# Performance work log

Hardware: AMD Instinct MI355X
Metric: run time of the kernel (lower is better)

## Reference

```python
import jax, jax.numpy as jnp
import numpy as np

# Mex config (matches init_kwargs)
B, C, H, W = 64, 64, 64, 64
BLK = (64, 3, 3)        # block over (C, H, W); spans all channels -> out_c = 1
STR = (64, 2, 2)
PAD = (0, 1, 1)
NI = 256                # num_instances
EPS = 1.0
SOFTMAX_MODE = False    # False -> mean (logsumexp - log k), True -> plain logsumexp


def setup_inputs() -> dict:
    key = jax.random.key(0)
    k1, k2 = jax.random.split(key)
    x = jax.random.normal(k1, (B, C, H, W), dtype=jnp.float32)
    kblk = BLK[0] * BLK[1] * BLK[2]
    # Dirichlet([1]*k) init == normalized exponentials; nregions = 1 (shared offsets)
    e = jax.random.exponential(k2, (1, NI, kblk), dtype=jnp.float32)
    offsets = (e / jnp.sum(e, axis=-1, keepdims=True)).reshape(1, NI, *BLK)
    return {"x": x, "offsets": offsets}


def _mex_forward(x, offsets):
    eps = jnp.float32(EPS)
    bc, bh, bw = BLK
    # im2col patch extraction: (B, C*bh*bw, OH, OW); feature dim ordered (c, fh, fw)
    patches = jax.lax.conv_general_dilated_patches(
        x, (bh, bw), (STR[1], STR[2]),
        [(PAD[1], PAD[1]), (PAD[2], PAD[2])],  # zero padding == blocks_out_of_bounds_value
        dimension_numbers=("NCHW", "OIHW", "NCHW"),
    )
    Bn, K, OH, OW = patches.shape  # K = bc*bh*bw = 576
    P = patches.transpose(0, 2, 3, 1).reshape(-1, K)  # (N, k), N = B*OH*OW
    O = offsets.reshape(NI, K)                         # single shared region

    # y_ni = (1/eps) * logsumexp_k( eps*(P_nk + O_ik) ) - log(k)/eps (mean mode)
    # exp-domain GEMM with max-shift for stability:
    Pe = eps * P
    Oe = eps * O
    mp = jnp.max(Pe, axis=1, keepdims=True)   # (N, 1)
    mo = jnp.max(Oe, axis=1, keepdims=True)   # (I, 1)
    S = jnp.exp(Pe - mp) @ jnp.exp(Oe - mo).T  # (N, I)
    y = (jnp.log(S) + mp + mo.T) / eps
    if not SOFTMAX_MODE:
        y = y - jnp.log(jnp.float32(K)) / eps
    # output: (B, num_instances * out_c, OH, OW) with out_c = 1
    return y.reshape(Bn, OH, OW, NI).transpose(0, 3, 1, 2)


def reference(x, offsets):
    return _mex_forward(x, offsets)
```

## Files before the change

### kernel.cpp

```cpp
#include <hip/hip_runtime.h>
#include <hip/hip_bf16.h>


typedef __bf16 bf16x8 __attribute__((ext_vector_type(8)));
typedef float  f32x4  __attribute__((ext_vector_type(4)));

#define GLD16(gp, lp) __builtin_amdgcn_global_load_lds(                        \
    (const __attribute__((address_space(1))) unsigned int*)(gp),               \
    (__attribute__((address_space(3))) unsigned int*)(lp), 16, 0, 0)

__global__ void mex_prep_b(const float* __restrict__ off, __bf16* __restrict__ Bt) {
    const int i = blockIdx.x * 4 + (threadIdx.x >> 6);
    const int c = threadIdx.x & 63;
    const float* oi = off + i * 576;
    __bf16* bi = Bt + i * 576;
    #pragma unroll
    for (int p = 0; p < 9; ++p) {
        float v = oi[c * 9 + p];
        bi[p * 64 + c] = (__bf16)__expf(v);
    }
}

__global__ __launch_bounds__(256) void mex_exp_tr(const float* __restrict__ x,
                                                  __bf16* __restrict__ E) {
    __shared__ __bf16 t[64 * 68];
    const int bh = blockIdx.x;
    const int b  = bh >> 6, h = bh & 63;
    const float* xp = x + ((size_t)b << 18) + (h << 6);
    const int tid = threadIdx.x;

    #pragma unroll
    for (int i = 0; i < 4; ++i) {
        const int f  = tid + i * 256;
        const int c  = f >> 4;
        const int w0 = (f & 15) << 2;
        float4 v = *(const float4*)(xp + c * 4096 + w0);
        __bf16* d = &t[c * 68 + w0];
        d[0] = (__bf16)__expf(v.x);
        d[1] = (__bf16)__expf(v.y);
        d[2] = (__bf16)__expf(v.z);
        d[3] = (__bf16)__expf(v.w);
    }
    __syncthreads();

    __bf16* Erow = E + ((size_t)bh << 12);
    #pragma unroll
    for (int j = 0; j < 2; ++j) {
        const int id = tid + j * 256;
        const int w = id >> 3, c8 = id & 7;
        bf16x8 v;
        #pragma unroll
        for (int ii = 0; ii < 8; ++ii) v[ii] = t[(c8 * 8 + ii) * 68 + w];
        const int c8p = c8 ^ ((w >> 1) & 7);
        *(bf16x8*)(Erow + w * 64 + c8p * 8) = v;
    }
}

__global__ __launch_bounds__(256, 3) void mex_main(
        const __bf16* __restrict__ E,
        const __bf16* __restrict__ Bt,
        float* __restrict__ out) {
    __shared__ bf16x8 lds8[5 * 66 * 8];

    const int bid = blockIdx.x;
    const int b   = bid >> 4;
    const int oh0 = (bid & 15) << 1;
    const int tid  = threadIdx.x;
    const int lane = tid & 63;
    const int wv   = tid >> 6;

    bf16x8 one8;
    #pragma unroll
    for (int j = 0; j < 8; ++j) one8[j] = (__bf16)1.0f;
    if (tid < 40) {
        const int hl = tid >> 3, cc = tid & 7;
        lds8[(hl * 66) * 8 + cc] = one8;
    }
    if (oh0 == 0) {
        for (int i = tid; i < 66 * 8; i += 256) lds8[i] = one8;
    }

    #pragma unroll
    for (int s = 0; s < 10; ++s) {
        const int seg = wv * 10 + s;
        const int hl = seg >> 3, sg = seg & 7;
        const int hg = 2 * oh0 - 1 + hl;
        if (hg >= 0) {
            const __bf16* gp = E + (((size_t)b * 64 + hg) << 12) + (sg << 9) + (lane << 3);
            bf16x8* lp = lds8 + hl * 528 + 8 + sg * 64;
            GLD16(gp, lp);
        }
    }
    __syncthreads();

    const int t16 = tid & 15;
    const int q   = (tid >> 4) & 3;

    int rbase[4], owv[4];
    #pragma unroll
    for (int mt = 0; mt < 4; ++mt) {
        const int m = mt * 16 + t16;
        owv[mt]   = m & 31;
        rbase[mt] = ((m >> 5) * 132) + ((m & 31) * 2);
    }

    const bf16x8* __restrict__ Btv = (const bf16x8*)Bt;
    const int instRow = (wv * 64 + t16) * 72 + q;

    f32x4 acc[4][4];
    #pragma unroll
    for (int mt = 0; mt < 4; ++mt)
        #pragma unroll
        for (int nt = 0; nt < 4; ++nt)
            acc[mt][nt] = (f32x4)(0.0f);

    bf16x8 bcur[4];
    #pragma unroll
    for (int nt = 0; nt < 4; ++nt)
        bcur[nt] = Btv[instRow + nt * (16 * 72)];

    #pragma unroll 2
    for (int ks = 0; ks < 18; ++ks) {
        const int p  = ks >> 1;
        const int fh = (p * 11) >> 5;
        const int fw = p - fh * 3;
        const int rofs = fh * 66 + fw;
        const int ccq  = ((ks & 1) << 2) + q;

        bf16x8 a[4];
        #pragma unroll
        for (int mt = 0; mt < 4; ++mt) {
            const int row = rbase[mt] + rofs;
            const int key = ((owv[mt] * 2 + fw - 1) >> 1) & 7;
            a[mt] = lds8[row * 8 + (ccq ^ key)];
        }

        bf16x8 bnext[4];
        if (ks < 17) {
            #pragma unroll
            for (int nt = 0; nt < 4; ++nt)
                bnext[nt] = Btv[instRow + nt * (16 * 72) + (ks + 1) * 4];
        }

        #pragma unroll
        for (int mt = 0; mt < 4; ++mt)
            #pragma unroll
            for (int nt = 0; nt < 4; ++nt)
                acc[mt][nt] = __builtin_amdgcn_mfma_f32_16x16x32_bf16(
                    a[mt], bcur[nt], acc[mt][nt], 0, 0, 0);

        #pragma unroll
        for (int nt = 0; nt < 4; ++nt) bcur[nt] = bnext[nt];
    }

    const float lK = 6.356107660695891f;
    #pragma unroll
    for (int mt = 0; mt < 4; ++mt) {
        const int m   = mt * 16 + (q << 2);
        const int ohl = m >> 5;
        const int owi = m & 31;
        const int orow = (oh0 + ohl) * 32 + owi;
        #pragma unroll
        for (int nt = 0; nt < 4; ++nt) {
            const int inst = wv * 64 + nt * 16 + t16;
            f32x4 r;
            #pragma unroll
            for (int j = 0; j < 4; ++j)
                r[j] = __logf(acc[mt][nt][j]) - lK;
            *(f32x4*)(out + (((size_t)b * 256 + inst) * 1024 + orow)) = r;
        }
    }
}

extern "C" void kernel_launch(void* const* d_in, const int* in_sizes, int n_in,
                              void* d_out, int out_size, void* d_ws, size_t ws_size,
                              hipStream_t stream) {
    const float* x   = (const float*)d_in[0];
    const float* off = (const float*)d_in[1];
    float* out = (float*)d_out;
    __bf16* E  = (__bf16*)d_ws;
    __bf16* Bt = (__bf16*)((char*)d_ws + 33554432);

    mex_prep_b<<<64, 256, 0, stream>>>(off, Bt);
    mex_exp_tr<<<4096, 256, 0, stream>>>(x, E);
    mex_main<<<1024, 256, 0, stream>>>(E, Bt, out);
}
```

Measured before the change: 157.1 us.

## Drop LDS transpose in exp kernel and swizzle block-to-XCD mapping

The exp/transpose kernel no longer stages data through LDS. Each wave loads eight channel-strided floats per lane, exponentiates them and writes one swizzled bf16x8 vector, on a grid reduced from 4096 to 512 blocks. Both the exp kernel and the main kernel remap block IDs with a (x - b) & 7 rotation over groups of eight, apparently to spread each batch's rows across the XCDs and improve L2 locality for the halo rows the main kernel reads. The main kernel also issues its first B-operand loads before the LDS fill, so those loads overlap the fill. The risk is that the strided 256-byte-per-wave global reads coalesce worse than the old float4 loads.

```diff
diff --git a/kernel.cpp b/kernel.cpp
--- a/kernel.cpp
+++ b/kernel.cpp
@@ -23,36 +23,26 @@
 
 __global__ __launch_bounds__(256) void mex_exp_tr(const float* __restrict__ x,
                                                   __bf16* __restrict__ E) {
-    __shared__ __bf16 t[64 * 68];
-    const int bh = blockIdx.x;
-    const int b  = bh >> 6, h = bh & 63;
-    const float* xp = x + ((size_t)b << 18) + (h << 6);
-    const int tid = threadIdx.x;
+    const int id = blockIdx.x;
+    const int b  = id >> 3;
+    const int g  = (id - b) & 7;
+    const int lane = threadIdx.x & 63;
+    const int wv   = threadIdx.x >> 6;
 
-    #pragma unroll
-    for (int i = 0; i < 4; ++i) {
-        const int f  = tid + i * 256;
-        const int c  = f >> 4;
-        const int w0 = (f & 15) << 2;
-        float4 v = *(const float4*)(xp + c * 4096 + w0);
-        __bf16* d = &t[c * 68 + w0];
-        d[0] = (__bf16)__expf(v.x);
-        d[1] = (__bf16)__expf(v.y);
-        d[2] = (__bf16)__expf(v.z);
-        d[3] = (__bf16)__expf(v.w);
-    }
-    __syncthreads();
-
-    __bf16* Erow = E + ((size_t)bh << 12);
-    #pragma unroll
-    for (int j = 0; j < 2; ++j) {
-        const int id = tid + j * 256;
-        const int w = id >> 3, c8 = id & 7;
-        bf16x8 v;
+    #pragma unroll 4
+    for (int tt = 0; tt < 16; ++tt) {
+        const int task = tt * 4 + wv;
+        const int hh = task >> 3, c8 = task & 7;
+        const int h  = g * 8 + hh;
+        const float* xp = x + (((size_t)(b * 64 + c8 * 8)) << 12) + (h << 6) + lane;
+        float v[8];
         #pragma unroll
-        for (int ii = 0; ii < 8; ++ii) v[ii] = t[(c8 * 8 + ii) * 68 + w];
-        const int c8p = c8 ^ ((w >> 1) & 7);
-        *(bf16x8*)(Erow + w * 64 + c8p * 8) = v;
+        for (int j = 0; j < 8; ++j) v[j] = xp[(size_t)j << 12];
+        bf16x8 o;
+        #pragma unroll
+        for (int j = 0; j < 8; ++j) o[j] = (__bf16)__expf(v[j]);
+        const int c8p = c8 ^ ((lane >> 1) & 7);
+        *(bf16x8*)(E + (((size_t)(b * 64 + h)) << 12) + (lane << 6) + (c8p << 3)) = o;
     }
 }
 
@@ -63,11 +53,25 @@
     __shared__ bf16x8 lds8[5 * 66 * 8];
 
     const int bid = blockIdx.x;
-    const int b   = bid >> 4;
-    const int oh0 = (bid & 15) << 1;
+    const int x8  = bid & 7;
+    const int tt  = bid >> 3;
+    const int b   = tt >> 1;
+    const int e   = tt & 1;
+    const int g   = (x8 - b) & 7;
+    const int oh0 = (g * 2 + e) * 2;
+
     const int tid  = threadIdx.x;
     const int lane = tid & 63;
     const int wv   = tid >> 6;
+    const int t16  = tid & 15;
+    const int q    = (tid >> 4) & 3;
+
+    const bf16x8* __restrict__ Btv = (const bf16x8*)Bt;
+    const int instRow = (wv * 64 + t16) * 72 + q;
+    bf16x8 bcur[4];
+    #pragma unroll
+    for (int nt = 0; nt < 4; ++nt)
+        bcur[nt] = Btv[instRow + nt * (16 * 72)];
 
     bf16x8 one8;
     #pragma unroll
@@ -93,9 +97,6 @@
     }
     __syncthreads();
 
-    const int t16 = tid & 15;
-    const int q   = (tid >> 4) & 3;
-
     int rbase[4], owv[4];
     #pragma unroll
     for (int mt = 0; mt < 4; ++mt) {
@@ -104,20 +105,12 @@
         rbase[mt] = ((m >> 5) * 132) + ((m & 31) * 2);
     }
 
-    const bf16x8* __restrict__ Btv = (const bf16x8*)Bt;
-    const int instRow = (wv * 64 + t16) * 72 + q;
-
     f32x4 acc[4][4];
     #pragma unroll
     for (int mt = 0; mt < 4; ++mt)
         #pragma unroll
         for (int nt = 0; nt < 4; ++nt)
             acc[mt][nt] = (f32x4)(0.0f);
-
-    bf16x8 bcur[4];
-    #pragma unroll
-    for (int nt = 0; nt < 4; ++nt)
-        bcur[nt] = Btv[instRow + nt * (16 * 72)];
 
     #pragma unroll 2
     for (int ks = 0; ks < 18; ++ks) {
@@ -182,6 +175,6 @@
     __bf16* Bt = (__bf16*)((char*)d_ws + 33554432);
 
     mex_prep_b<<<64, 256, 0, stream>>>(off, Bt);
-    mex_exp_tr<<<4096, 256, 0, stream>>>(x, E);
+    mex_exp_tr<<<512, 256, 0, stream>>>(x, E);
     mex_main<<<1024, 256, 0, stream>>>(E, Bt, out);
 }
```

Result: slower. 165.1 us (+5.1%).
